# Kernel optimization log

Measured on AMD Instinct MI355X. Metric: run time of the kernel, lower is better.

Reference implementation:

```python
import jax, jax.numpy as jnp
import numpy as np

N_NODES = 50000
N_EDGES = 800000
N_GRAPHS = 64
F_IN = 128
HEADS = 4
CH = 32
HID = HEADS * CH  # 128
N_CLASSES = 10
N_LAYERS = 3
NEG_SLOPE = 0.2


def setup_inputs() -> dict:
    key = jax.random.key(0)
    ks = jax.random.split(key, 12)
    x = jax.random.normal(ks[0], (N_NODES, F_IN), dtype=jnp.float32)
    edge_index = jax.random.randint(ks[1], (2, N_EDGES), 0, N_NODES, dtype=jnp.int64)
    batch = jnp.sort(jax.random.randint(ks[2], (N_NODES,), 0, N_GRAPHS, dtype=jnp.int64))
    s = 0.1
    Wl = jax.random.normal(ks[3], (N_LAYERS, F_IN, HID), dtype=jnp.float32) * s
    Wr = jax.random.normal(ks[4], (N_LAYERS, F_IN, HID), dtype=jnp.float32) * s
    bl = jax.random.normal(ks[5], (N_LAYERS, HID), dtype=jnp.float32) * s
    br = jax.random.normal(ks[6], (N_LAYERS, HID), dtype=jnp.float32) * s
    att = jax.random.normal(ks[7], (N_LAYERS, HEADS, CH), dtype=jnp.float32) * s
    bias = jax.random.normal(ks[8], (N_LAYERS, HID), dtype=jnp.float32) * s
    lin_w = jax.random.normal(ks[9], (HID, N_CLASSES), dtype=jnp.float32) * s
    lin_b = jax.random.normal(ks[10], (N_CLASSES,), dtype=jnp.float32) * s
    return {"x": x, "edge_index": edge_index, "batch": batch, "Wl": Wl, "Wr": Wr,
            "bl": bl, "br": br, "att": att, "bias": bias, "lin_w": lin_w, "lin_b": lin_b}


def gatv2_layer(x, Wl, Wr, bl, br, att, bias, src, dst):
    # x: [N, D_in] -> out: [N, HEADS*CH]
    n = x.shape[0]
    xl = (x @ Wl + bl).reshape(n, HEADS, CH)  # source transform
    xr = (x @ Wr + br).reshape(n, HEADS, CH)  # target transform
    # GATv2 edge scores: a^T LeakyReLU(W_l x_j + W_r x_i), per head
    e = jnp.einsum('ehc,hc->eh', jax.nn.leaky_relu(xl[src] + xr[dst], NEG_SLOPE), att)  # [E, H]
    # softmax over edges sharing the same destination node
    m = jax.ops.segment_max(e, dst, num_segments=n)
    ee = jnp.exp(e - m[dst])
    denom = jax.ops.segment_sum(ee, dst, num_segments=n)
    alpha = ee / denom[dst]  # [E, H]
    out = jax.ops.segment_sum(xl[src] * alpha[:, :, None], dst, num_segments=n)  # [N, H, C]
    return out.reshape(n, HID) + bias


def reference(x, edge_index, batch, Wl, Wr, bl, br, att, bias, lin_w, lin_b):
    n = x.shape[0]
    loop = jnp.arange(n, dtype=edge_index.dtype)
    src = jnp.concatenate([edge_index[0], loop])  # self loops (PyG default)
    dst = jnp.concatenate([edge_index[1], loop])
    h = x
    for l in range(N_LAYERS):
        h = jax.nn.elu(gatv2_layer(h, Wl[l], Wr[l], bl[l], br[l], att[l], bias[l], src, dst))
    # global mean pool over graphs
    sums = jax.ops.segment_sum(h, batch, num_segments=N_GRAPHS)
    cnt = jax.ops.segment_sum(jnp.ones((n,), h.dtype), batch, num_segments=N_GRAPHS)
    pooled = sums / jnp.maximum(cnt, 1.0)[:, None]
    logits = jax.nn.elu(pooled @ lin_w + lin_b)
    return jax.nn.log_softmax(logits, axis=1)
```

## Files before the change

kernel.cpp:

```cpp
#include <hip/hip_runtime.h>
#include <hip/hip_bf16.h>
#include <math.h>

#define N_NODES 50000
#define N_EDGES 800000
#define N_GRAPHS 64
#define HID 128
#define N_CLASSES 10
#define N_LAYERS 3
#define NEG_SLOPE 0.2f

#define NB 196
#define BCAP 5120
#define ACHUNK 4096

typedef __attribute__((ext_vector_type(8))) short short8;
typedef __attribute__((ext_vector_type(4))) float f32x4;
typedef __attribute__((ext_vector_type(2))) _Float16 h2;

__device__ inline ushort f2bf(float f) {
    uint u = __builtin_bit_cast(uint, f);
    u += 0x7fffu + ((u >> 16) & 1u);
    return (ushort)(u >> 16);
}
__device__ inline uint pk2bf(float a, float b) {
    return (uint)f2bf(a) | ((uint)f2bf(b) << 16);
}
__device__ inline h2 pkh(float a, float b) {
    return __builtin_bit_cast(h2, __builtin_amdgcn_cvt_pkrtz(a, b));
}


__global__ __launch_bounds__(256) void setup_kernel(
    const float* __restrict__ x, uint* __restrict__ xb, int n,
    const float* __restrict__ Wl, const float* __restrict__ Wr,
    uint* __restrict__ wt, int wtot,
    const int* __restrict__ ei, int E,
    int* __restrict__ bptr, uint* __restrict__ bbuf,
    int xqb, int wb) {
    __shared__ int hcnt[256];
    __shared__ int hexcl[256];
    __shared__ int lofs[256];
    __shared__ int delta[256];
    __shared__ uint stage[ACHUNK];
    int t = threadIdx.x;
    int blk = blockIdx.x;

    if (blk < xqb) {
        int j = blk * 256 + t;
        if (j < n * 16) {
            const float4* xp = (const float4*)x + (size_t)j * 2;
            float4 a = xp[0], b = xp[1];
            uint4 o;
            o.x = pk2bf(a.x, a.y); o.y = pk2bf(a.z, a.w);
            o.z = pk2bf(b.x, b.y); o.w = pk2bf(b.z, b.w);
            ((uint4*)xb)[j] = o;
        }
        return;
    }
    blk -= xqb;
    if (blk < wb) {
        int i = blk * 256 + t;
        if (i >= wtot) return;
        int kp = i & 63;
        int nn = (i >> 6) & 255;
        int l  = i >> 14;
        const float* W = (nn < 128) ? Wl : Wr;
        int c = nn & 127;
        wt[i] = pk2bf(W[l * 16384 + (2 * kp) * 128 + c],
                      W[l * 16384 + (2 * kp + 1) * 128 + c]);
        return;
    }
    blk -= wb;
    int total = E + n;
    int base = blk * ACHUNK;
    int cntblk = min(ACHUNK, total - base);
    hcnt[t] = 0; lofs[t] = 0;
    __syncthreads();

    uint v[16]; int bk[16];
#pragma unroll
    for (int j = 0; j < 16; ++j) {
        int e = base + j * 256 + t;
        bk[j] = -1;
        if (e < total) {
            int s, d;
            if (e < E) { s = ei[e]; d = ei[E + e]; }
            else       { s = e - E; d = e - E; }
            v[j] = ((uint)s << 16) | (uint)d;
            bk[j] = d >> 8;
            atomicAdd(&hcnt[bk[j]], 1);
        }
    }
    __syncthreads();
    int hv = hcnt[t];
    __shared__ int stmp[256];
    stmp[t] = hv;
    __syncthreads();
    for (int off = 1; off < 256; off <<= 1) {
        int u = (t >= off) ? stmp[t - off] : 0;
        __syncthreads();
        stmp[t] += u;
        __syncthreads();
    }
    hexcl[t] = stmp[t] - hv;
    __syncthreads();
#pragma unroll
    for (int j = 0; j < 16; ++j) {
        if (bk[j] >= 0) {
            int pos = hexcl[bk[j]] + atomicAdd(&lofs[bk[j]], 1);
            stage[pos] = v[j];
        }
    }
    __syncthreads();
    if (t < NB) {
        int c = hcnt[t];
        int gb = c ? atomicAdd(&bptr[t], c) : 0;
        delta[t] = t * BCAP + gb - hexcl[t];
    }
    __syncthreads();
    for (int idx = t; idx < cntblk; idx += 256) {
        uint val = stage[idx];
        int b = (val >> 8) & 0xff;
        int tgt = delta[b] + idx;
        if (tgt < (b + 1) * BCAP) bbuf[tgt] = val;
    }
}


__device__ __forceinline__ void gemm_body(
    const ushort* __restrict__ A, const ushort* __restrict__ Wt,
    const float* __restrict__ bl, const float* __restrict__ br,
    ushort* __restrict__ xlb, ushort* __restrict__ xrb, int n, int bid, int tid) {
    int wv = tid >> 6;
    int lane = tid & 63;
    int q = lane >> 4, m16 = lane & 15;
    int m0 = bid * 64;

    short8 bf[4][4];
#pragma unroll
    for (int nt = 0; nt < 4; ++nt) {
        const ushort* wp = Wt + (size_t)(wv * 64 + nt * 16 + m16) * 128 + q * 8;
#pragma unroll
        for (int ks = 0; ks < 4; ++ks) bf[nt][ks] = *(const short8*)(wp + ks * 32);
    }
    const ushort* ap[4];
#pragma unroll
    for (int mt = 0; mt < 4; ++mt) {
        int r = m0 + mt * 16 + m16;
        if (r > n - 1) r = n - 1;
        ap[mt] = A + (size_t)r * 128 + q * 8;
    }

    f32x4 z = {0.f, 0.f, 0.f, 0.f};
    f32x4 acc[4][4];
#pragma unroll
    for (int mt = 0; mt < 4; ++mt)
#pragma unroll
        for (int nt = 0; nt < 4; ++nt) acc[mt][nt] = z;

#pragma unroll
    for (int ks = 0; ks < 4; ++ks) {
        short8 af[4];
#pragma unroll
        for (int mt = 0; mt < 4; ++mt) af[mt] = *(const short8*)(ap[mt] + ks * 32);
#pragma unroll
        for (int mt = 0; mt < 4; ++mt)
#pragma unroll
            for (int nt = 0; nt < 4; ++nt)
                acc[mt][nt] = __builtin_amdgcn_mfma_f32_16x16x32_bf16(
                    bf[nt][ks], af[mt], acc[mt][nt], 0, 0, 0);
    }

    ushort* outp = (wv >= 2) ? xrb : xlb;
    const float* bx = (wv >= 2) ? br : bl;
    int fb = (wv & 1) * 64;
#pragma unroll
    for (int nt = 0; nt < 4; ++nt) {
        int fcol = fb + nt * 16 + q * 4;
        float4 b4 = *(const float4*)&bx[fcol];
#pragma unroll
        for (int mt = 0; mt < 4; ++mt) {
            int m = m0 + mt * 16 + m16;
            if (m < n) {
                uint2 pk;
                pk.x = __builtin_bit_cast(uint, pkh(acc[mt][nt][0] + b4.x,
                                                    acc[mt][nt][1] + b4.y));
                pk.y = __builtin_bit_cast(uint, pkh(acc[mt][nt][2] + b4.z,
                                                    acc[mt][nt][3] + b4.w));
                *(uint2*)&outp[(size_t)m * 128 + fcol] = pk;
            }
        }
    }
}

__global__ __launch_bounds__(256) void csr_gemm0_kernel(
    const int* __restrict__ bptr, const uint* __restrict__ bbuf, int n,
    int* __restrict__ row_start, int* __restrict__ ssrc,
    const ushort* __restrict__ A, const ushort* __restrict__ Wt,
    const float* __restrict__ bl, const float* __restrict__ br,
    ushort* __restrict__ xlb, ushort* __restrict__ xrb) {
    int t = threadIdx.x;
    if (blockIdx.x >= NB) {
        gemm_body(A, Wt, bl, br, xlb, xrb, n, blockIdx.x - NB, t);
        return;
    }
    int b = blockIdx.x;
    __shared__ int sb[256], h[256], hx[256], lofs[256];
    int bv = (t < NB) ? min(bptr[t], BCAP) : 0;
    sb[t] = bv;
    __syncthreads();
    for (int off = 1; off < 256; off <<= 1) {
        int u = (t >= off) ? sb[t - off] : 0;
        __syncthreads();
        sb[t] += u;
        __syncthreads();
    }
    int cnt = min(bptr[b], BCAP);
    int base = sb[b] - cnt;
    if (b == NB - 1 && t == 0) row_start[n] = sb[NB - 1];
    h[t] = 0; lofs[t] = 0;
    __syncthreads();
    const uint* bp = bbuf + (size_t)b * BCAP;
    for (int k = t; k < cnt; k += 256) atomicAdd(&h[bp[k] & 255u], 1);
    __syncthreads();
    int hv = h[t];
    hx[t] = hv;
    __syncthreads();
    for (int off = 1; off < 256; off <<= 1) {
        int u = (t >= off) ? hx[t - off] : 0;
        __syncthreads();
        hx[t] += u;
        __syncthreads();
    }
    int excl = hx[t] - hv;
    int node = (b << 8) + t;
    if (node < n) row_start[node] = base + excl;
    __syncthreads();
    h[t] = excl;
    __syncthreads();
    for (int k = t; k < cnt; k += 256) {
        uint val = bp[k];
        int dl = val & 255u;
        int pos = base + h[dl] + atomicAdd(&lofs[dl], 1);
        ssrc[pos] = (int)((val & 0xffff0000u) >> 8);
    }
}

__global__ __launch_bounds__(256) void gemm_mfma(
    const ushort* __restrict__ A, const ushort* __restrict__ Wt,
    const float* __restrict__ bl, const float* __restrict__ br,
    ushort* __restrict__ xlb, ushort* __restrict__ xrb, int n) {
    gemm_body(A, Wt, bl, br, xlb, xrb, n, blockIdx.x, threadIdx.x);
}


#define SLOT(u, u01, u23, e0)                              \
    h2 u01 = __builtin_bit_cast(h2, u.x);                  \
    h2 u23 = __builtin_bit_cast(h2, u.y);                  \
    float e0;                                              \
    {                                                      \
        h2 t01 = u01 + xr01, t23 = u23 + xr23;             \
        t01 = __builtin_elementwise_max(t01, t01 * K02);   \
        t23 = __builtin_elementwise_max(t23, t23 * K02);   \
        h2 eh = EINIT;                                     \
        eh += at01 * t01;                                  \
        eh += at23 * t23;                                  \
        e0 = (float)(_Float16)(eh.x + eh.y);               \
    }

__global__ __launch_bounds__(256) void attn_kernel(
    const uint* __restrict__ xlb, const uint* __restrict__ xrb,
    const float* __restrict__ att, const float* __restrict__ bias,
    const int* __restrict__ row_start, const int* __restrict__ ssrc,
    uint* __restrict__ hout, int n) {
    int wave = threadIdx.x >> 6;
    int lane = threadIdx.x & 63;
    int half = lane >> 5;
    int l32  = lane & 31;
    int i = blockIdx.x * 4 + wave;
    if (i >= n) return;

    const char* xlB = (const char*)xlb;
    int lofs = l32 * 8;

    uint2 xru = *(const uint2*)((const char*)xrb + (size_t)i * 256 + lofs);
    h2 xr01 = __builtin_bit_cast(h2, xru.x);
    h2 xr23 = __builtin_bit_cast(h2, xru.y);
    const float L2E = 1.4426950408889634f;
    float4 at = ((const float4*)att)[l32];
    h2 at01 = pkh(at.x * L2E, at.y * L2E);
    h2 at23 = pkh(at.z * L2E, at.w * L2E);
    const h2 K02   = {(_Float16)0.2f, (_Float16)0.2f};
    const h2 EINIT = {(_Float16)-0.5f, (_Float16)-0.5f};

    int p0 = row_start[i], p1 = row_start[i + 1];

    float den0 = 0.f, den1 = 0.f;
    h2 aA01 = {0, 0}, aA23 = {0, 0};
    h2 aB01 = {0, 0}, aB23 = {0, 0};

    int p = p0;
    for (; p + 8 <= p1; p += 8) {
        uint s0 = (uint)ssrc[p + half];
        uint s1 = (uint)ssrc[p + 2 + half];
        uint s2 = (uint)ssrc[p + 4 + half];
        uint s3 = (uint)ssrc[p + 6 + half];
        uint2 u0 = *(const uint2*)(xlB + (size_t)s0 + lofs);
        uint2 u1 = *(const uint2*)(xlB + (size_t)s1 + lofs);
        uint2 u2 = *(const uint2*)(xlB + (size_t)s2 + lofs);
        uint2 u3 = *(const uint2*)(xlB + (size_t)s3 + lofs);
        SLOT(u0, v001, v023, e0);
        SLOT(u1, v101, v123, e1);
        SLOT(u2, v201, v223, e2);
        SLOT(u3, v301, v323, e3);
        e0 += __shfl_xor(e0, 1); e1 += __shfl_xor(e1, 1);
        e2 += __shfl_xor(e2, 1); e3 += __shfl_xor(e3, 1);
        e0 += __shfl_xor(e0, 2); e1 += __shfl_xor(e1, 2);
        e2 += __shfl_xor(e2, 2); e3 += __shfl_xor(e3, 2);
        e0 += __shfl_xor(e0, 4); e1 += __shfl_xor(e1, 4);
        e2 += __shfl_xor(e2, 4); e3 += __shfl_xor(e3, 4);
        float w0 = exp2f(e0), w1 = exp2f(e1), w2 = exp2f(e2), w3 = exp2f(e3);
        den0 += w0 + w2; den1 += w1 + w3;
        h2 wh0 = pkh(w0, w0), wh1 = pkh(w1, w1);
        h2 wh2 = pkh(w2, w2), wh3 = pkh(w3, w3);
        aA01 += wh0 * v001; aA23 += wh0 * v023;
        aB01 += wh1 * v101; aB23 += wh1 * v123;
        aA01 += wh2 * v201; aA23 += wh2 * v223;
        aB01 += wh3 * v301; aB23 += wh3 * v323;
    }
    if (p + 4 <= p1) {
        uint s0 = (uint)ssrc[p + half];
        uint s1 = (uint)ssrc[p + 2 + half];
        uint2 u0 = *(const uint2*)(xlB + (size_t)s0 + lofs);
        uint2 u1 = *(const uint2*)(xlB + (size_t)s1 + lofs);
        SLOT(u0, v001, v023, e0);
        SLOT(u1, v101, v123, e1);
        e0 += __shfl_xor(e0, 1); e1 += __shfl_xor(e1, 1);
        e0 += __shfl_xor(e0, 2); e1 += __shfl_xor(e1, 2);
        e0 += __shfl_xor(e0, 4); e1 += __shfl_xor(e1, 4);
        float w0 = exp2f(e0), w1 = exp2f(e1);
        den0 += w0; den1 += w1;
        h2 wh0 = pkh(w0, w0), wh1 = pkh(w1, w1);
        aA01 += wh0 * v001; aA23 += wh0 * v023;
        aB01 += wh1 * v101; aB23 += wh1 * v123;
        p += 4;
    }
    if (p < p1) {
        int eA = p + half, eB = p + 2 + half;
        int lst = p1 - 1;
        uint s0 = (uint)ssrc[min(eA, lst)];
        uint s1 = (uint)ssrc[min(eB, lst)];
        uint2 u0 = *(const uint2*)(xlB + (size_t)s0 + lofs);
        uint2 u1 = *(const uint2*)(xlB + (size_t)s1 + lofs);
        SLOT(u0, v001, v023, e0);
        SLOT(u1, v101, v123, e1);
        e0 += __shfl_xor(e0, 1); e1 += __shfl_xor(e1, 1);
        e0 += __shfl_xor(e0, 2); e1 += __shfl_xor(e1, 2);
        e0 += __shfl_xor(e0, 4); e1 += __shfl_xor(e1, 4);
        float w0 = (eA < p1) ? exp2f(e0) : 0.f;
        float w1 = (eB < p1) ? exp2f(e1) : 0.f;
        den0 += w0; den1 += w1;
        h2 wh0 = pkh(w0, w0), wh1 = pkh(w1, w1);
        aA01 += wh0 * v001; aA23 += wh0 * v023;
        aB01 += wh1 * v101; aB23 += wh1 * v123;
    }

    float den = den0 + den1;
    float a0 = (float)(_Float16)(aA01.x + aB01.x);
    float a1 = (float)(_Float16)(aA01.y + aB01.y);
    float a2 = (float)(_Float16)(aA23.x + aB23.x);
    float a3 = (float)(_Float16)(aA23.y + aB23.y);
    den += __shfl_xor(den, 32);
    a0 += __shfl_xor(a0, 32);
    a1 += __shfl_xor(a1, 32);
    a2 += __shfl_xor(a2, 32);
    a3 += __shfl_xor(a3, 32);

    if (half == 0) {
        float inv = 1.f / den;
        float4 bi = ((const float4*)bias)[l32];
        float o0 = a0 * inv + bi.x; o0 = o0 > 0.f ? o0 : __expf(o0) - 1.f;
        float o1 = a1 * inv + bi.y; o1 = o1 > 0.f ? o1 : __expf(o1) - 1.f;
        float o2 = a2 * inv + bi.z; o2 = o2 > 0.f ? o2 : __expf(o2) - 1.f;
        float o3 = a3 * inv + bi.w; o3 = o3 > 0.f ? o3 : __expf(o3) - 1.f;
        uint2 pk;
        pk.x = pk2bf(o0, o1);
        pk.y = pk2bf(o2, o3);
        *(uint2*)((char*)hout + (size_t)i * 256 + lofs) = pk;
    }
}


__device__ inline float bflo(uint v) { return __builtin_bit_cast(float, v << 16); }
__device__ inline float bfhi(uint v) { return __builtin_bit_cast(float, v & 0xffff0000u); }

__global__ __launch_bounds__(256) void pool_kernel(const uint* __restrict__ h2v,
                                                   const int* __restrict__ batch, int n,
                                                   float* __restrict__ psum) {
    int g = blockIdx.x;
    int t = threadIdx.x;
    int cp = t & 63;
    int sub = (t >> 6) | (blockIdx.y << 2);
    int b, e;
    {
        int lo = 0, hi = n;
        while (lo < hi) { int mid = (lo + hi) >> 1; if (batch[mid] < g) lo = mid + 1; else hi = mid; }
        b = lo;
        lo = 0; hi = n;
        int g1 = g + 1;
        while (lo < hi) { int mid = (lo + hi) >> 1; if (batch[mid] < g1) lo = mid + 1; else hi = mid; }
        e = lo;
    }
    float a0 = 0.f, a1 = 0.f;
    for (int i = b + sub; i < e; i += 32) {
        uint u = h2v[(size_t)i * 64 + cp];
        a0 += bflo(u); a1 += bfhi(u);
    }
    __shared__ float r0[256], r1[256];
    r0[t] = a0; r1[t] = a1;
    __syncthreads();
    if (t < 64) {
        float s0 = r0[t] + r0[t + 64] + r0[t + 128] + r0[t + 192];
        float s1 = r1[t] + r1[t + 64] + r1[t + 128] + r1[t + 192];
        atomicAdd(&psum[g * 128 + 2 * t], s0);
        atomicAdd(&psum[g * 128 + 2 * t + 1], s1);
    }
}

__global__ void final_kernel(const float* __restrict__ psum, const int* __restrict__ batch,
                             int n, const float* __restrict__ lw,
                             const float* __restrict__ lb, float* __restrict__ out) {
    int g = threadIdx.x;
    if (g >= N_GRAPHS) return;
    int b, e;
    {
        int lo = 0, hi = n;
        while (lo < hi) { int mid = (lo + hi) >> 1; if (batch[mid] < g) lo = mid + 1; else hi = mid; }
        b = lo;
        lo = 0; hi = n;
        int g1 = g + 1;
        while (lo < hi) { int mid = (lo + hi) >> 1; if (batch[mid] < g1) lo = mid + 1; else hi = mid; }
        e = lo;
    }
    float invc = 1.f / fmaxf((float)(e - b), 1.f);
    float z[N_CLASSES];
#pragma unroll
    for (int c = 0; c < N_CLASSES; ++c) z[c] = lb[c];
    for (int k = 0; k < 128; ++k) {
        float p = psum[g * 128 + k] * invc;
#pragma unroll
        for (int c = 0; c < N_CLASSES; ++c) z[c] += p * lw[k * N_CLASSES + c];
    }
    float mx = -1e30f;
#pragma unroll
    for (int c = 0; c < N_CLASSES; ++c) {
        z[c] = z[c] > 0.f ? z[c] : expf(z[c]) - 1.f;
        mx = fmaxf(mx, z[c]);
    }
    float s = 0.f;
#pragma unroll
    for (int c = 0; c < N_CLASSES; ++c) s += expf(z[c] - mx);
    float lse = mx + logf(s);
#pragma unroll
    for (int c = 0; c < N_CLASSES; ++c) out[g * N_CLASSES + c] = z[c] - lse;
}


extern "C" void kernel_launch(void* const* d_in, const int* in_sizes, int n_in,
                              void* d_out, int out_size, void* d_ws, size_t ws_size,
                              hipStream_t stream) {
    const float* x     = (const float*)d_in[0];
    const int*   ei    = (const int*)d_in[1];
    const int*   batch = (const int*)d_in[2];
    const float* Wl    = (const float*)d_in[3];
    const float* Wr    = (const float*)d_in[4];
    const float* bl    = (const float*)d_in[5];
    const float* br    = (const float*)d_in[6];
    const float* att   = (const float*)d_in[7];
    const float* bias  = (const float*)d_in[8];
    const float* lw    = (const float*)d_in[9];
    const float* lb    = (const float*)d_in[10];
    float* out = (float*)d_out;

    const int n = in_sizes[2];
    const int E = in_sizes[1] / 2;
    const int total_edges = E + n;

    char* ws = (char*)d_ws;
    size_t o = 0;
    auto alloc = [&](size_t bytes) -> void* {
        void* p = ws + o;
        o = (o + bytes + 255) & ~(size_t)255;
        return p;
    };
    int*    row_start = (int*)alloc((size_t)(n + 1) * 4);
    int*    bptr      = (int*)alloc((size_t)NB * 4);
    uint*   bbuf      = (uint*)alloc((size_t)NB * BCAP * 4);
    int*    ssrc      = (int*)alloc((size_t)total_edges * 4);
    ushort* xbf0      = (ushort*)alloc((size_t)n * HID * 2);
    ushort* xlb       = (ushort*)alloc((size_t)n * HID * 2);
    ushort* xrb       = (ushort*)alloc((size_t)n * HID * 2);
    ushort* hbA       = (ushort*)alloc((size_t)n * HID * 2);
    ushort* hbB       = (ushort*)alloc((size_t)n * HID * 2);
    uint*   wt        = (uint*)alloc((size_t)N_LAYERS * 256 * 64 * 4);
    float*  psum      = (float*)alloc((size_t)N_GRAPHS * HID * 4);

    hipMemsetAsync(bptr, 0, (size_t)NB * 4, stream);
    hipMemsetAsync(psum, 0, (size_t)N_GRAPHS * HID * 4, stream);

    int wtot = N_LAYERS * 256 * 64;
    int xqb = (n * 16 + 255) / 256;
    int wb  = (wtot + 255) / 256;
    int pb  = (total_edges + ACHUNK - 1) / ACHUNK;
    setup_kernel<<<xqb + wb + pb, 256, 0, stream>>>(
        x, (uint*)xbf0, n, Wl, Wr, wt, wtot, ei, E, bptr, bbuf, xqb, wb);

    int mblocks = (n + 63) / 64;
    int ablocks = (n + 3) / 4;

    csr_gemm0_kernel<<<NB + mblocks, 256, 0, stream>>>(
        bptr, bbuf, n, row_start, ssrc,
        xbf0, (const ushort*)wt, bl, br, xlb, xrb);

    attn_kernel<<<ablocks, 256, 0, stream>>>((const uint*)xlb, (const uint*)xrb,
                                             att, bias, row_start, ssrc, (uint*)hbA, n);
    gemm_mfma<<<mblocks, 256, 0, stream>>>(hbA, (const ushort*)(wt + (size_t)256 * 64),
                                           bl + HID, br + HID, xlb, xrb, n);
    attn_kernel<<<ablocks, 256, 0, stream>>>((const uint*)xlb, (const uint*)xrb,
                                             att + HID, bias + HID, row_start, ssrc,
                                             (uint*)hbB, n);
    gemm_mfma<<<mblocks, 256, 0, stream>>>(hbB, (const ushort*)(wt + (size_t)2 * 256 * 64),
                                           bl + 2 * HID, br + 2 * HID, xlb, xrb, n);
    attn_kernel<<<ablocks, 256, 0, stream>>>((const uint*)xlb, (const uint*)xrb,
                                             att + 2 * HID, bias + 2 * HID, row_start, ssrc,
                                             (uint*)hbA, n);

    pool_kernel<<<dim3(N_GRAPHS, 8), 256, 0, stream>>>((const uint*)hbA, batch, n, psum);
    final_kernel<<<1, 64, 0, stream>>>(psum, batch, n, lw, lb, out);
}
```

Baseline: 341.0 us.

## Use packed half-precision score reduction and f16 exp2 in attention; drop pooling atomics

Edge scores in the attention kernel now stay in packed FP16. Two edges' scores are packed into one register, so each cross-lane shuffle reduces two edges at once, and exp2 and the denominator accumulation run in half precision. The 4-edge and remainder tails are merged into one masked 8-edge tail. The pooling kernel writes per-blockIdx.y partial sums instead of using float atomics, which removes the psum memset, and the final kernel sums the 8 partials. This cuts shuffle and conversion work and atomic traffic, at the cost of lower precision in the softmax weights and denominator. It also depends on the pooling grid having exactly 8 y-blocks.

```diff
diff --git a/kernel.cpp b/kernel.cpp
--- a/kernel.cpp
+++ b/kernel.cpp
@@ -17,6 +17,8 @@
 typedef __attribute__((ext_vector_type(8))) short short8;
 typedef __attribute__((ext_vector_type(4))) float f32x4;
 typedef __attribute__((ext_vector_type(2))) _Float16 h2;
+
+extern "C" __device__ _Float16 __ocml_exp2_f16(_Float16);
 
 __device__ inline ushort f2bf(float f) {
     uint u = __builtin_bit_cast(uint, f);
@@ -255,19 +257,28 @@
 }
 
 
-#define SLOT(u, u01, u23, e0)                              \
+#define SLOTE(u, u01, u23, eh)                             \
     h2 u01 = __builtin_bit_cast(h2, u.x);                  \
     h2 u23 = __builtin_bit_cast(h2, u.y);                  \
-    float e0;                                              \
+    h2 eh;                                                 \
     {                                                      \
         h2 t01 = u01 + xr01, t23 = u23 + xr23;             \
         t01 = __builtin_elementwise_max(t01, t01 * K02);   \
         t23 = __builtin_elementwise_max(t23, t23 * K02);   \
-        h2 eh = EINIT;                                     \
-        eh += at01 * t01;                                  \
+        eh = EINIT + at01 * t01;                           \
         eh += at23 * t23;                                  \
-        e0 = (float)(_Float16)(eh.x + eh.y);               \
-    }
+    }
+
+__device__ inline uint packpair(h2 a, h2 b) {
+    h2 lo = {a.x, b.x};
+    h2 hi = {a.y, b.y};
+    return __builtin_bit_cast(uint, lo + hi);
+}
+__device__ inline uint shfl_add_h2(uint q, int m) {
+    uint r = (uint)__shfl_xor((int)q, m);
+    h2 s = __builtin_bit_cast(h2, q) + __builtin_bit_cast(h2, r);
+    return __builtin_bit_cast(uint, s);
+}
 
 __global__ __launch_bounds__(256) void attn_kernel(
     const uint* __restrict__ xlb, const uint* __restrict__ xrb,
@@ -296,7 +307,7 @@
 
     int p0 = row_start[i], p1 = row_start[i + 1];
 
-    float den0 = 0.f, den1 = 0.f;
+    h2 denP = {0, 0};
     h2 aA01 = {0, 0}, aA23 = {0, 0};
     h2 aB01 = {0, 0}, aB23 = {0, 0};
 
@@ -310,63 +321,66 @@
         uint2 u1 = *(const uint2*)(xlB + (size_t)s1 + lofs);
         uint2 u2 = *(const uint2*)(xlB + (size_t)s2 + lofs);
         uint2 u3 = *(const uint2*)(xlB + (size_t)s3 + lofs);
-        SLOT(u0, v001, v023, e0);
-        SLOT(u1, v101, v123, e1);
-        SLOT(u2, v201, v223, e2);
-        SLOT(u3, v301, v323, e3);
-        e0 += __shfl_xor(e0, 1); e1 += __shfl_xor(e1, 1);
-        e2 += __shfl_xor(e2, 1); e3 += __shfl_xor(e3, 1);
-        e0 += __shfl_xor(e0, 2); e1 += __shfl_xor(e1, 2);
-        e2 += __shfl_xor(e2, 2); e3 += __shfl_xor(e3, 2);
-        e0 += __shfl_xor(e0, 4); e1 += __shfl_xor(e1, 4);
-        e2 += __shfl_xor(e2, 4); e3 += __shfl_xor(e3, 4);
-        float w0 = exp2f(e0), w1 = exp2f(e1), w2 = exp2f(e2), w3 = exp2f(e3);
-        den0 += w0 + w2; den1 += w1 + w3;
-        h2 wh0 = pkh(w0, w0), wh1 = pkh(w1, w1);
-        h2 wh2 = pkh(w2, w2), wh3 = pkh(w3, w3);
-        aA01 += wh0 * v001; aA23 += wh0 * v023;
-        aB01 += wh1 * v101; aB23 += wh1 * v123;
-        aA01 += wh2 * v201; aA23 += wh2 * v223;
-        aB01 += wh3 * v301; aB23 += wh3 * v323;
-    }
-    if (p + 4 <= p1) {
-        uint s0 = (uint)ssrc[p + half];
-        uint s1 = (uint)ssrc[p + 2 + half];
+        SLOTE(u0, v001, v023, eh0);
+        SLOTE(u1, v101, v123, eh1);
+        SLOTE(u2, v201, v223, eh2);
+        SLOTE(u3, v301, v323, eh3);
+        uint q01 = packpair(eh0, eh1);
+        uint q23 = packpair(eh2, eh3);
+        q01 = shfl_add_h2(q01, 1); q23 = shfl_add_h2(q23, 1);
+        q01 = shfl_add_h2(q01, 2); q23 = shfl_add_h2(q23, 2);
+        q01 = shfl_add_h2(q01, 4); q23 = shfl_add_h2(q23, 4);
+        h2 e01 = __builtin_bit_cast(h2, q01);
+        h2 e23 = __builtin_bit_cast(h2, q23);
+        h2 w01, w23;
+        w01.x = __ocml_exp2_f16(e01.x); w01.y = __ocml_exp2_f16(e01.y);
+        w23.x = __ocml_exp2_f16(e23.x); w23.y = __ocml_exp2_f16(e23.y);
+        denP += w01; denP += w23;
+        h2 wA = {w01.x, w01.x}, wB = {w01.y, w01.y};
+        h2 wC = {w23.x, w23.x}, wD = {w23.y, w23.y};
+        aA01 += wA * v001; aA23 += wA * v023;
+        aB01 += wB * v101; aB23 += wB * v123;
+        aA01 += wC * v201; aA23 += wC * v223;
+        aB01 += wD * v301; aB23 += wD * v323;
+    }
+    if (p < p1) {
+        int lst = p1 - 1;
+        int i0 = p + half, i1 = p + 2 + half, i2 = p + 4 + half, i3 = p + 6 + half;
+        uint s0 = (uint)ssrc[min(i0, lst)];
+        uint s1 = (uint)ssrc[min(i1, lst)];
+        uint s2 = (uint)ssrc[min(i2, lst)];
+        uint s3 = (uint)ssrc[min(i3, lst)];
         uint2 u0 = *(const uint2*)(xlB + (size_t)s0 + lofs);
         uint2 u1 = *(const uint2*)(xlB + (size_t)s1 + lofs);
-        SLOT(u0, v001, v023, e0);
-        SLOT(u1, v101, v123, e1);
-        e0 += __shfl_xor(e0, 1); e1 += __shfl_xor(e1, 1);
-        e0 += __shfl_xor(e0, 2); e1 += __shfl_xor(e1, 2);
-        e0 += __shfl_xor(e0, 4); e1 += __shfl_xor(e1, 4);
-        float w0 = exp2f(e0), w1 = exp2f(e1);
-        den0 += w0; den1 += w1;
-        h2 wh0 = pkh(w0, w0), wh1 = pkh(w1, w1);
-        aA01 += wh0 * v001; aA23 += wh0 * v023;
-        aB01 += wh1 * v101; aB23 += wh1 * v123;
-        p += 4;
-    }
-    if (p < p1) {
-        int eA = p + half, eB = p + 2 + half;
-        int lst = p1 - 1;
-        uint s0 = (uint)ssrc[min(eA, lst)];
-        uint s1 = (uint)ssrc[min(eB, lst)];
-        uint2 u0 = *(const uint2*)(xlB + (size_t)s0 + lofs);
-        uint2 u1 = *(const uint2*)(xlB + (size_t)s1 + lofs);
-        SLOT(u0, v001, v023, e0);
-        SLOT(u1, v101, v123, e1);
-        e0 += __shfl_xor(e0, 1); e1 += __shfl_xor(e1, 1);
-        e0 += __shfl_xor(e0, 2); e1 += __shfl_xor(e1, 2);
-        e0 += __shfl_xor(e0, 4); e1 += __shfl_xor(e1, 4);
-        float w0 = (eA < p1) ? exp2f(e0) : 0.f;
-        float w1 = (eB < p1) ? exp2f(e1) : 0.f;
-        den0 += w0; den1 += w1;
-        h2 wh0 = pkh(w0, w0), wh1 = pkh(w1, w1);
-        aA01 += wh0 * v001; aA23 += wh0 * v023;
-        aB01 += wh1 * v101; aB23 += wh1 * v123;
-    }
-
-    float den = den0 + den1;
+        uint2 u2 = *(const uint2*)(xlB + (size_t)s2 + lofs);
+        uint2 u3 = *(const uint2*)(xlB + (size_t)s3 + lofs);
+        SLOTE(u0, v001, v023, eh0);
+        SLOTE(u1, v101, v123, eh1);
+        SLOTE(u2, v201, v223, eh2);
+        SLOTE(u3, v301, v323, eh3);
+        uint q01 = packpair(eh0, eh1);
+        uint q23 = packpair(eh2, eh3);
+        q01 = shfl_add_h2(q01, 1); q23 = shfl_add_h2(q23, 1);
+        q01 = shfl_add_h2(q01, 2); q23 = shfl_add_h2(q23, 2);
+        q01 = shfl_add_h2(q01, 4); q23 = shfl_add_h2(q23, 4);
+        h2 e01 = __builtin_bit_cast(h2, q01);
+        h2 e23 = __builtin_bit_cast(h2, q23);
+        h2 w01, w23;
+        const _Float16 zh = (_Float16)0.f;
+        w01.x = (i0 < p1) ? __ocml_exp2_f16(e01.x) : zh;
+        w01.y = (i1 < p1) ? __ocml_exp2_f16(e01.y) : zh;
+        w23.x = (i2 < p1) ? __ocml_exp2_f16(e23.x) : zh;
+        w23.y = (i3 < p1) ? __ocml_exp2_f16(e23.y) : zh;
+        denP += w01; denP += w23;
+        h2 wA = {w01.x, w01.x}, wB = {w01.y, w01.y};
+        h2 wC = {w23.x, w23.x}, wD = {w23.y, w23.y};
+        aA01 += wA * v001; aA23 += wA * v023;
+        aB01 += wB * v101; aB23 += wB * v123;
+        aA01 += wC * v201; aA23 += wC * v223;
+        aB01 += wD * v301; aB23 += wD * v323;
+    }
+
+    float den = (float)denP.x + (float)denP.y;
     float a0 = (float)(_Float16)(aA01.x + aB01.x);
     float a1 = (float)(_Float16)(aA01.y + aB01.y);
     float a2 = (float)(_Float16)(aA23.x + aB23.x);
@@ -423,8 +437,9 @@
     if (t < 64) {
         float s0 = r0[t] + r0[t + 64] + r0[t + 128] + r0[t + 192];
         float s1 = r1[t] + r1[t + 64] + r1[t + 128] + r1[t + 192];
-        atomicAdd(&psum[g * 128 + 2 * t], s0);
-        atomicAdd(&psum[g * 128 + 2 * t + 1], s1);
+        float* pp = &psum[((size_t)blockIdx.y * 64 + g) * 128];
+        pp[2 * t]     = s0;
+        pp[2 * t + 1] = s1;
     }
 }
 
@@ -448,7 +463,10 @@
 #pragma unroll
     for (int c = 0; c < N_CLASSES; ++c) z[c] = lb[c];
     for (int k = 0; k < 128; ++k) {
-        float p = psum[g * 128 + k] * invc;
+        float p = 0.f;
+#pragma unroll
+        for (int y = 0; y < 8; ++y) p += psum[((size_t)y * 64 + g) * 128 + k];
+        p *= invc;
 #pragma unroll
         for (int c = 0; c < N_CLASSES; ++c) z[c] += p * lw[k * N_CLASSES + c];
     }
@@ -504,10 +522,9 @@
     ushort* hbA       = (ushort*)alloc((size_t)n * HID * 2);
     ushort* hbB       = (ushort*)alloc((size_t)n * HID * 2);
     uint*   wt        = (uint*)alloc((size_t)N_LAYERS * 256 * 64 * 4);
-    float*  psum      = (float*)alloc((size_t)N_GRAPHS * HID * 4);
+    float*  psum      = (float*)alloc((size_t)8 * N_GRAPHS * HID * 4);
 
     hipMemsetAsync(bptr, 0, (size_t)NB * 4, stream);
-    hipMemsetAsync(psum, 0, (size_t)N_GRAPHS * HID * 4, stream);
 
     int wtot = N_LAYERS * 256 * 64;
     int xqb = (n * 16 + 255) / 256;
```

After: 351.0 us. 2.9% more time.
